# Kernel tuning notes

Measured on AMD Instinct MI355X. Metric: run time of the kernel, lower is better.

## Reference

```python
import jax, jax.numpy as jnp
import numpy as np

IMAGE_SIZE = 640
NUM_CLASSES = 80
MAX_BOXES = 100
SCORE_THR = 0.25
IOU_THR = 0.1
K_PRE = 256  # pre-NMS candidates per class (fixed-shape surrogate for tf.where filtering)
ANCHORS = np.array([[10,13],[16,30],[33,23],[30,61],[62,45],[59,119],
                    [116,90],[156,198],[373,326]], dtype=np.float32)


def setup_inputs() -> dict:
    key = jax.random.key(0)
    k5, k4, k3 = jax.random.split(key, 3)
    B = 16
    return {
        "p5": jax.random.normal(k5, (B, 20, 20, 255), dtype=jnp.float32),
        "p4": jax.random.normal(k4, (B, 40, 40, 255), dtype=jnp.float32),
        "p3": jax.random.normal(k3, (B, 80, 80, 255), dtype=jnp.float32),
    }


def _decode_layer(fm, anchors):
    # fm: [B, g, g, 3*(5+C)]; anchors: [3, 2] in input-image pixels
    B, g = fm.shape[0], fm.shape[1]
    ratio = IMAGE_SIZE / g
    fm = fm.reshape(B, g, g, 3, 5 + NUM_CLASSES)
    ctr = jax.nn.sigmoid(fm[..., :2])                      # [B,g,g,3,2]
    gx, gy = jnp.meshgrid(jnp.arange(g), jnp.arange(g))    # 'xy' indexing, same as tf
    offset = jnp.stack([gx, gy], axis=-1).astype(fm.dtype)[:, :, None, :]
    ctr = (ctr + offset) * ratio                           # pixel-space centers (x, y)
    # (anchor/ratio)*exp(t)*ratio == anchor*exp(t)
    sizes = jnp.exp(fm[..., 2:4]) * anchors                # pixel-space (w, h)
    conf = jax.nn.sigmoid(fm[..., 4:5])
    prob = jax.nn.sigmoid(fm[..., 5:])
    boxes = jnp.concatenate([ctr, sizes], axis=-1).reshape(B, -1, 4)
    scores = (conf * prob).reshape(B, -1, NUM_CLASSES)
    return boxes, scores


def _pairwise_iou(b):
    # b: [K, 4] in (x1, y1, x2, y2)
    x1, y1, x2, y2 = b[:, 0], b[:, 1], b[:, 2], b[:, 3]
    area = jnp.maximum(x2 - x1, 0.0) * jnp.maximum(y2 - y1, 0.0)
    iw = jnp.maximum(jnp.minimum(x2[:, None], x2[None, :]) - jnp.maximum(x1[:, None], x1[None, :]), 0.0)
    ih = jnp.maximum(jnp.minimum(y2[:, None], y2[None, :]) - jnp.maximum(y1[:, None], y1[None, :]), 0.0)
    inter = iw * ih
    union = area[:, None] + area[None, :] - inter
    return inter / jnp.maximum(union, 1e-9)


def _nms_class(boxes, scores):
    # boxes: [N,4], scores: [N] for one class of one image
    s = jnp.where(scores > SCORE_THR, scores, -1.0)
    top_s, top_i = jax.lax.top_k(s, K_PRE)        # score-sorted candidates
    cb = jnp.take(boxes, top_i, axis=0)           # [K_PRE, 4]
    iou = _pairwise_iou(cb)                       # [K_PRE, K_PRE]
    idx = jnp.arange(K_PRE)
    supp0 = top_s <= SCORE_THR                    # below-threshold slots start suppressed

    def body(i, supp):
        alive = ~supp[i]
        return supp | (alive & (iou[i] > IOU_THR) & (idx > i))

    supp = jax.lax.fori_loop(0, K_PRE, body, supp0)
    keep = ~supp
    # tf NMS caps output at MAX_BOXES per class (boxes are score-sorted)
    keep = keep & (jnp.cumsum(keep.astype(jnp.int32)) <= MAX_BOXES)
    kept_s = jnp.where(keep, top_s, -1.0)
    return kept_s, top_i


def _nms_image(boxes, scores):
    # boxes: [N,4], scores: [N,C]
    kept_s, top_i = jax.vmap(_nms_class, in_axes=(None, 1))(boxes, scores)  # [C,K],[C,K]
    flat_s = kept_s.reshape(-1)
    flat_i = top_i.reshape(-1)
    cls = jnp.repeat(jnp.arange(NUM_CLASSES), K_PRE)
    fs, fi = jax.lax.top_k(flat_s, MAX_BOXES)     # global top-k across all classes
    box_idx = flat_i[fi]
    valid = fs > 0.0                              # padded/suppressed slots carry -1
    out_boxes = jnp.where(valid[:, None], jnp.take(boxes, box_idx, axis=0), -1.0)
    out_scores = jnp.where(valid, fs, -1.0)
    out_labels = jnp.where(valid, cls[fi], -1).astype(jnp.int32)
    return out_boxes, out_scores, out_labels


def reference(p5, p4, p3):
    b5, s5 = _decode_layer(p5, ANCHORS[6:9])
    b4, s4 = _decode_layer(p4, ANCHORS[3:6])
    b3, s3 = _decode_layer(p3, ANCHORS[0:3])
    boxes = jnp.concatenate([b5, b4, b3], axis=1)   # [B, 25200, 4] (cx, cy, w, h)
    scores = jnp.concatenate([s5, s4, s3], axis=1)  # [B, 25200, 80]
    cx, cy, w, h = boxes[..., 0], boxes[..., 1], boxes[..., 2], boxes[..., 3]
    boxes = jnp.stack([cx - w / 2, cy - h / 2, cx + w / 2, cy + h / 2], axis=-1)
    return jax.vmap(_nms_image)(boxes, scores)      # ([B,100,4], [B,100], [B,100] int32)
```

## Files before the change

kernel.cpp:

```cpp
#include <hip/hip_runtime.h>
#include <cstdint>

#define NBOX 25200
#define NCLS 80
#define NIMG 16
#define KPRE 256
#define MAXB 100
#define SCORE_THR 0.25f
#define IOU_THR 0.1f
#define GCAP 512
#define GCAP_OLD 2048
#define NBINS_OLD 4096
#define FK 512
#define LCAP 3072
#define SCAP 24
#define CSTR 16
#define CUT 0.5f
#define BINW 0.001953125f
#define HS2 512.0f
#define RSC 262144.0f
#define BPI 394
#define FBBINS 2048

__constant__ float c_AW[9] = {10.f,16.f,33.f,30.f,62.f,59.f,116.f,156.f,373.f};
__constant__ float c_AH[9] = {13.f,30.f,23.f,61.f,45.f,119.f,90.f,198.f,326.f};

__device__ __forceinline__ float sigmoidf_(float x) { return 1.0f / (1.0f + expf(-x)); }

__device__ __forceinline__ void box_loc(int i, const float* p5, const float* p4, const float* p3,
                                        const float*& p, int& g, int& li, int& abase) {
  if (i < 1200)      { p = p5; g = 20; li = i;        abase = 6; }
  else if (i < 6000) { p = p4; g = 40; li = i - 1200; abase = 3; }
  else               { p = p3; g = 80; li = i - 6000; abase = 0; }
}

__device__ __forceinline__ float score_full(const float* p5, const float* p4, const float* p3,
                                            int b, int c, int i) {
  const float* p; int g, li, abase;
  box_loc(i, p5, p4, p3, p, g, li, abase);
  const float* f = p + (size_t)((size_t)b * g * g * 3 + li) * 85;
  return __fmul_rn(sigmoidf_(f[4]), sigmoidf_(f[5 + c]));
}

__global__ __launch_bounds__(512) void decode_push_kernel(
    const float* __restrict__ p5, const float* __restrict__ p4, const float* __restrict__ p3,
    float* __restrict__ boxes, unsigned long long* __restrict__ lists,
    uint32_t* __restrict__ cnts, uint32_t* __restrict__ ovfl)
{
  __shared__ float rec[64 * 85];
  __shared__ float conf_s[64];
  __shared__ unsigned long long slist[NCLS][SCAP];
  __shared__ uint32_t wcnt[NCLS];
  __shared__ uint32_t sbase[NCLS], sst[NCLS];

  const int bi = blockIdx.x;
  const int b = bi / BPI, r = bi - b * BPI;
  const float* p; int g, lb, s0, nb, abase;
  if (r < 19)      { p = p5; g = 20; lb = 0;    s0 = r * 64;        abase = 6; nb = 1200  - s0; }
  else if (r < 94) { p = p4; g = 40; lb = 1200; s0 = (r - 19) * 64; abase = 3; nb = 4800  - s0; }
  else             { p = p3; g = 80; lb = 6000; s0 = (r - 94) * 64; abase = 0; nb = 19200 - s0; }
  if (nb > 64) nb = 64;
  const int tid = threadIdx.x;

  {
    const float4* src4 = (const float4*)(p + ((size_t)b * g * g * 3 + s0) * 85);
    float4* rec4 = (float4*)rec;
    int n4 = nb * 85 / 4;
    for (int k = tid; k < n4; k += 512) rec4[k] = src4[k];
  }
  __syncthreads();

  if (tid < nb) {
    const float* f = rec + tid * 85;
    int li = s0 + tid;
    int cell = li / 3, a = li - cell * 3;
    float ratio = 640.0f / (float)g;
    float cx = (sigmoidf_(f[0]) + (float)(cell % g)) * ratio;
    float cy = (sigmoidf_(f[1]) + (float)(cell / g)) * ratio;
    float w = expf(f[2]) * c_AW[abase + a];
    float h = expf(f[3]) * c_AH[abase + a];
    float hw = 0.5f * w, hh = 0.5f * h;
    float4* ob = (float4*)(boxes + ((size_t)b * NBOX + lb + li) * 4);
    *ob = make_float4(cx - hw, cy - hh, cx + hw, cy + hh);
    conf_s[tid] = sigmoidf_(f[4]);
  }
  __syncthreads();

  {
    const int wave = tid >> 6, lane = tid & 63;
    const int c0 = wave * 10;
    const bool jok = lane < nb;
    const float cf = jok ? conf_s[lane] : 0.0f;
    const uint32_t gidx = (uint32_t)(lb + s0 + lane);
    const float* fl = rec + lane * 85 + 5;
    const unsigned long long lt = (lane == 0) ? 0ull : (~0ull >> (64 - lane));
    for (int cc = 0; cc < 10; ++cc) {
      int c = c0 + cc;
      float s = 0.0f;
      if (jok) s = __fmul_rn(cf, sigmoidf_(fl[c]));
      bool pred = jok && (s > CUT);
      unsigned long long m = __ballot(pred);
      uint32_t pc = (uint32_t)__popcll(m);
      if (pred) {
        uint32_t rank = (uint32_t)__popcll(m & lt);
        if (rank < SCAP)
          slist[c][rank] = ((unsigned long long)__float_as_uint(s) << 32) | (0xFFFFFFFFu - gidx);
      }
      if (lane == 0) {
        wcnt[c] = pc;
        if (pc > SCAP) ovfl[b * NCLS + c] = 1u;
      }
    }
  }
  __syncthreads();

  if (tid < NCLS) {
    uint32_t full = wcnt[tid];
    uint32_t st = full < SCAP ? full : SCAP;
    sst[tid] = st;
    sbase[tid] = atomicAdd(&cnts[(size_t)(b * NCLS + tid) * CSTR], st);
  }
  __syncthreads();

  for (int t = tid; t < NCLS * SCAP; t += 512) {
    int c = t / SCAP, k = t - c * SCAP;
    if ((uint32_t)k < sst[c]) {
      uint32_t dst = sbase[c] + (uint32_t)k;
      if (dst < LCAP)
        lists[(size_t)(b * NCLS + c) * LCAP + dst] = slist[c][k];
    }
  }
}

union ShMix2 {
  uint32_t rhist[512];
  uint32_t fhist[FBBINS];
  unsigned long long rowm[KPRE][4];
};

__global__ __launch_bounds__(512) void select_nms_list_kernel(
    const unsigned long long* __restrict__ lists, const uint32_t* __restrict__ cnts,
    const uint32_t* __restrict__ ovfl, const float* __restrict__ boxes,
    const float* __restrict__ p5, const float* __restrict__ p4, const float* __restrict__ p3,
    float* __restrict__ kept_s, int* __restrict__ top_i)
{
  const int task = blockIdx.x;
  const int b = task / NCLS, c = task - b * NCLS;
  const int tid = threadIdx.x;

  __shared__ uint32_t S[256];
  __shared__ unsigned long long keys[GCAP];
  __shared__ ShMix2 u;
  __shared__ float4 bbx[KPRE];
  __shared__ float bar_[KPRE];
  __shared__ unsigned long long suppInit[4];
  __shared__ unsigned long long sh_t[4];
  __shared__ int s_B, s_cnt, s_state, sh_stop;
  __shared__ float s_gl, s_lo, s_hi;
  __shared__ uint32_t s_above, s_g2;

  const uint32_t cntraw = cnts[(size_t)task * CSTR];
  bool fb = (ovfl[task] != 0u) || !(cntraw >= (uint32_t)KPRE && cntraw <= (uint32_t)LCAP);
  float thr = CUT;
  int n_all = (int)(cntraw < (uint32_t)LCAP ? cntraw : (uint32_t)LCAP);
  const unsigned long long* gl = lists + (size_t)task * LCAP;

  if (!fb) {
    if (tid < 256) S[tid] = 0;
    __syncthreads();
    for (int z = tid; z < n_all; z += 512) {
      float s = __uint_as_float((uint32_t)(gl[z] >> 32));
      int bin = (int)(__fmul_rn(__fsub_rn(s, CUT), HS2));
      bin = bin < 0 ? 0 : (bin > 255 ? 255 : bin);
      atomicAdd(&S[bin], 1u);
    }
    __syncthreads();
    for (int off = 1; off < 256; off <<= 1) {
      uint32_t add = 0;
      if (tid < 256 && tid + off < 256) add = S[tid + off];
      __syncthreads();
      if (tid < 256) S[tid] += add;
      __syncthreads();
    }
    if (tid == 0) s_B = 0;
    __syncthreads();
    if (tid < 256) {
      uint32_t Sz = S[tid];
      uint32_t Sz1 = (tid < 255) ? S[tid + 1] : 0u;
      if (Sz >= KPRE && (tid == 255 || Sz1 < KPRE)) s_B = tid;
    }
    __syncthreads();
    const int B = s_B;
    const uint32_t gcount = S[B];
    const uint32_t aboveB = (B < 255) ? S[B + 1] : 0u;
    thr = CUT + (float)B * BINW;
    if (gcount > 500u) {
      for (int z = tid; z < 512; z += 512) u.rhist[z] = 0u;
      __syncthreads();
      float rLo = thr;
      for (int z = tid; z < n_all; z += 512) {
        float s = __uint_as_float((uint32_t)(gl[z] >> 32));
        int bin = (int)(__fmul_rn(__fsub_rn(s, CUT), HS2));
        bin = bin < 0 ? 0 : (bin > 255 ? 255 : bin);
        if (bin == B) {
          int sub = (int)((s - rLo) * RSC);
          sub = sub < 0 ? 0 : (sub > 511 ? 511 : sub);
          atomicAdd(&u.rhist[sub], 1u);
        }
      }
      __syncthreads();
      if (tid == 0) {
        uint32_t acc = aboveB; int B2 = 0;
        for (int z = 511; z >= 0; --z) {
          acc += u.rhist[z];
          if (acc >= KPRE) { B2 = z; break; }
        }
        s_gl = rLo + (float)B2 * (BINW / 512.0f);
        s_g2 = acc;
      }
      __syncthreads();
      thr = s_gl;
      if (s_g2 > 500u) fb = true;
      __syncthreads();
    }
  }

  if (fb) {
    float lo = SCORE_THR, hi = 1.0f;
    uint32_t above = 0;
    float gl2 = SCORE_THR;
    bool done = false;
    for (int iter = 0; iter < 6 && !done; ++iter) {
      for (int z = tid; z < FBBINS; z += 512) u.fhist[z] = 0u;
      __syncthreads();
      float scale = (float)FBBINS / (hi - lo);
      for (int i = tid; i < NBOX; i += 512) {
        float s = score_full(p5, p4, p3, b, c, i);
        if (s > lo && s <= hi) {
          int bin = (int)((s - lo) * scale);
          bin = bin < 0 ? 0 : (bin > FBBINS - 1 ? FBBINS - 1 : bin);
          atomicAdd(&u.fhist[bin], 1u);
        }
      }
      __syncthreads();
      if (tid < 256) {
        uint32_t cs = 0; int base = tid * 8;
        #pragma unroll
        for (int z = 0; z < 8; ++z) cs += u.fhist[base + z];
        S[tid] = cs;
      }
      __syncthreads();
      if (tid == 0) {
        uint32_t acc = 0; int ch;
        for (ch = 255; ch >= 0; --ch) {
          if (above + acc + S[ch] >= KPRE) break;
          acc += S[ch];
        }
        if (ch < 0) { s_state = 1; s_gl = SCORE_THR; }
        else {
          int B = -1;
          for (int z = ch * 8 + 7; z >= ch * 8; --z) {
            acc += u.fhist[z];
            if (above + acc >= KPRE) { B = z; break; }
          }
          uint32_t popB = u.fhist[B];
          uint32_t aboveNew = above + acc - popB;
          float wdt = (hi - lo) / (float)FBBINS;
          float binLo = lo + (float)B * wdt;
          if (aboveNew + popB <= 496u || iter == 5) { s_state = 1; s_gl = binLo; }
          else { s_state = 0; s_lo = binLo; s_hi = binLo + wdt; s_above = aboveNew; }
        }
      }
      __syncthreads();
      if (s_state == 1) { gl2 = s_gl; done = true; }
      else { lo = s_lo; hi = s_hi; above = s_above; }
      __syncthreads();
    }
    thr = gl2;
  }

  float thr_n = __uint_as_float(__float_as_uint(thr) - 8u);

  if (tid == 0) s_cnt = 0;
  __syncthreads();
  if (!fb) {
    for (int z = tid; z < n_all; z += 512) {
      unsigned long long kk = gl[z];
      float s = __uint_as_float((uint32_t)(kk >> 32));
      if (s > thr_n) {
        int slot = atomicAdd(&s_cnt, 1);
        if (slot < GCAP) keys[slot] = kk;
      }
    }
  } else {
    for (int i = tid; i < NBOX; i += 512) {
      float s = score_full(p5, p4, p3, b, c, i);
      if (s > thr_n && s > SCORE_THR) {
        int slot = atomicAdd(&s_cnt, 1);
        if (slot < GCAP)
          keys[slot] = ((unsigned long long)__float_as_uint(s) << 32) | (0xFFFFFFFFu - (uint32_t)i);
      }
    }
  }
  __syncthreads();
  int n = s_cnt < GCAP ? s_cnt : GCAP;
  if (tid >= n) keys[tid] = 0ull;
  __syncthreads();
  for (int k = 2; k <= GCAP; k <<= 1) {
    for (int j = k >> 1; j > 0; j >>= 1) {
      int ixj = tid ^ j;
      if (ixj > tid) {
        unsigned long long a0 = keys[tid], b0_ = keys[ixj];
        bool sw = ((tid & k) == 0) ? (a0 < b0_) : (a0 > b0_);
        if (sw) { keys[tid] = b0_; keys[ixj] = a0; }
      }
      __syncthreads();
    }
  }

  const int col = tid & 255;
  float sc; int idx;
  {
    unsigned long long kk = keys[col];
    if ((uint32_t)(kk >> 32) != 0u) { sc = __uint_as_float((uint32_t)(kk >> 32)); idx = (int)(0xFFFFFFFFu - (uint32_t)kk); }
    else { sc = -1.0f; idx = 0; }
  }
  if (tid < KPRE) {
    const float* bp = boxes + ((size_t)b * NBOX + idx) * 4;
    float bx1 = bp[0], by1 = bp[1], bx2 = bp[2], by2 = bp[3];
    bbx[tid] = make_float4(bx1, by1, bx2, by2);
    bar_[tid] = __fmul_rn(fmaxf(__fsub_rn(bx2, bx1), 0.0f), fmaxf(__fsub_rn(by2, by1), 0.0f));
  }
  {
    unsigned long long alive = __ballot(sc > SCORE_THR);
    if (tid < KPRE && (tid & 63) == 0) suppInit[tid >> 6] = ~alive;
  }
  if (tid == 0) sh_stop = 0;
  __syncthreads();
  float4 MB = bbx[col];
  float x1 = MB.x, y1 = MB.y, x2 = MB.z, y2 = MB.w;
  float area = bar_[col];
  if (tid < 4) sh_t[tid] = suppInit[tid];
  __syncthreads();

  int P = 4;
  const int rg = tid >> 8;
  #pragma unroll
  for (int q = 0; q < 4; ++q) {
    for (int ii = 0; ii < 64; ii += 2) {
      int i = q * 64 + ii + rg;
      if (!((sh_t[q] >> (ii + rg)) & 1ull)) {
        float4 B = bbx[i];
        float ar = bar_[i];
        float iw = fmaxf(__fsub_rn(fminf(x2, B.z), fmaxf(x1, B.x)), 0.0f);
        float ih = fmaxf(__fsub_rn(fminf(y2, B.w), fmaxf(y1, B.y)), 0.0f);
        float inter = __fmul_rn(iw, ih);
        float ab = __fadd_rn(ar, area);
        float diff = __fsub_rn(__fmul_rn(inter, 1.1f), __fmul_rn(0.1f, ab));
        bool sup;
        if (fabsf(diff) > 1e-5f * ab) {
          sup = diff > 0.0f;
        } else {
          float uni = __fsub_rn(ab, inter);
          sup = (inter / fmaxf(uni, 1e-9f)) > IOU_THR;
        }
        sup = sup && (col > i);
        unsigned long long m = __ballot(sup);
        if ((tid & 63) == 0) u.rowm[i][(tid >> 6) & 3] = m;
      }
    }
    __syncthreads();
    if (tid == 0) {
      unsigned long long t0 = sh_t[0], t1 = sh_t[1], t2 = sh_t[2], t3 = sh_t[3];
      for (int ii = 0; ii < 64; ++ii) {
        int i = q * 64 + ii;
        unsigned long long cur = (q == 0) ? t0 : (q == 1) ? t1 : (q == 2) ? t2 : t3;
        if (!((cur >> ii) & 1ull)) {
          if (q <= 0) t0 |= u.rowm[i][0];
          if (q <= 1) t1 |= u.rowm[i][1];
          if (q <= 2) t2 |= u.rowm[i][2];
          t3 |= u.rowm[i][3];
        }
      }
      sh_t[0] = t0; sh_t[1] = t1; sh_t[2] = t2; sh_t[3] = t3;
      int kept = __popcll(~t0);
      if (q >= 1) kept += __popcll(~t1);
      if (q >= 2) kept += __popcll(~t2);
      if (q >= 3) kept += __popcll(~t3);
      if (kept >= MAXB) sh_stop = 1;
    }
    __syncthreads();
    if (sh_stop) { P = q + 1; break; }
  }

  if (tid < KPRE) {
    unsigned long long tw = sh_t[tid >> 6];
    bool kept = (tid < 64 * P) && !((tw >> (tid & 63)) & 1ull);
    int rank = 0;
    #pragma unroll
    for (int w2 = 0; w2 < 4; ++w2)
      if (w2 < (tid >> 6)) rank += __popcll(~sh_t[w2]);
    int l = tid & 63;
    rank += (l == 0) ? 0 : __popcll(~tw & ((~0ull) >> (64 - l)));
    bool fin = kept && (rank < MAXB);
    kept_s[(size_t)task * KPRE + tid] = fin ? sc : -1.0f;
    top_i[(size_t)task * KPRE + tid] = idx;
  }
}

__global__ __launch_bounds__(256) void decode_kernel(
    const float* __restrict__ p5, const float* __restrict__ p4, const float* __restrict__ p3,
    float* __restrict__ boxes, float* __restrict__ conf)
{
  int t = blockIdx.x * 256 + threadIdx.x;
  if (t >= NIMG * NBOX) return;
  int b = t / NBOX, i = t - b * NBOX;
  const float* p; int g, li, abase;
  box_loc(i, p5, p4, p3, p, g, li, abase);
  int cell = li / 3, a = li - cell * 3;
  float ratio = 640.0f / (float)g;
  const float* f = p + ((size_t)((size_t)b * g * g + cell) * 255 + a * 85);
  float cx = (sigmoidf_(f[0]) + (float)(cell % g)) * ratio;
  float cy = (sigmoidf_(f[1]) + (float)(cell / g)) * ratio;
  float w = expf(f[2]) * c_AW[abase + a];
  float h = expf(f[3]) * c_AH[abase + a];
  float hw = 0.5f * w, hh = 0.5f * h;
  float* ob = boxes + (size_t)t * 4;
  ob[0] = cx - hw; ob[1] = cy - hh; ob[2] = cx + hw; ob[3] = cy + hh;
  conf[t] = sigmoidf_(f[4]);
}

__device__ __forceinline__ float score_at(
    const float* __restrict__ p5, const float* __restrict__ p4, const float* __restrict__ p3,
    const float* __restrict__ conf, int b, int c, int i)
{
  const float* p; int g, li, abase;
  box_loc(i, p5, p4, p3, p, g, li, abase);
  float logit = p[(size_t)((size_t)b * g * g * 3 + li) * 85 + 5 + c];
  return __fmul_rn(conf[b * NBOX + i], 1.0f / (1.0f + expf(-logit)));
}

__global__ __launch_bounds__(256) void select_nms_kernel(
    const float* __restrict__ p5, const float* __restrict__ p4, const float* __restrict__ p3,
    const float* __restrict__ conf, const float* __restrict__ boxes,
    float* __restrict__ kept_s, int* __restrict__ top_i)
{
  const int task = blockIdx.x;
  const int b = task / NCLS, c = task - b * NCLS;
  const int tid = threadIdx.x;
  __shared__ uint32_t hist[NBINS_OLD];
  __shared__ uint32_t chunkS[256];
  __shared__ unsigned long long keys[GCAP_OLD];
  __shared__ float s_lo, s_hi, s_glo;
  __shared__ uint32_t s_above;
  __shared__ int s_state, s_cnt;

  float lo = SCORE_THR, hi = 1.0f;
  uint32_t above = 0;
  float gatherLo = SCORE_THR;
  bool done = false;
  for (int iter = 0; iter < 6 && !done; ++iter) {
    for (int z = tid; z < NBINS_OLD; z += 256) hist[z] = 0;
    __syncthreads();
    float scale = (float)NBINS_OLD / (hi - lo);
    for (int i = tid; i < NBOX; i += 256) {
      float s = score_at(p5, p4, p3, conf, b, c, i);
      if (s > lo && s <= hi) {
        int bin = (int)((s - lo) * scale);
        bin = bin < 0 ? 0 : (bin > NBINS_OLD - 1 ? NBINS_OLD - 1 : bin);
        atomicAdd(&hist[bin], 1u);
      }
    }
    __syncthreads();
    { uint32_t cs = 0; int base = tid * 16;
      #pragma unroll
      for (int z = 0; z < 16; ++z) cs += hist[base + z];
      chunkS[tid] = cs; }
    __syncthreads();
    if (tid == 0) {
      uint32_t acc = 0; int ch;
      for (ch = 255; ch >= 0; --ch) {
        if (above + acc + chunkS[ch] >= KPRE) break;
        acc += chunkS[ch];
      }
      if (ch < 0) { s_state = 1; s_glo = SCORE_THR; }
      else {
        int B = -1;
        for (int z = ch * 16 + 15; z >= ch * 16; --z) {
          acc += hist[z];
          if (above + acc >= KPRE) { B = z; break; }
        }
        uint32_t popB = hist[B];
        uint32_t aboveNew = above + acc - popB;
        float wdt = (hi - lo) / (float)NBINS_OLD;
        float binLo = lo + (float)B * wdt;
        if (aboveNew + popB <= 1024u || iter == 5) { s_state = 1; s_glo = binLo; }
        else { s_state = 0; s_lo = binLo; s_hi = binLo + wdt; s_above = aboveNew; }
      }
    }
    __syncthreads();
    if (s_state == 1) { gatherLo = s_glo; done = true; }
    else { lo = s_lo; hi = s_hi; above = s_above; }
    __syncthreads();
  }
  gatherLo = __uint_as_float(__float_as_uint(gatherLo) - 8u);
  if (tid == 0) s_cnt = 0;
  __syncthreads();
  for (int i = tid; i < NBOX; i += 256) {
    float s = score_at(p5, p4, p3, conf, b, c, i);
    if (s > gatherLo && s > SCORE_THR) {
      int slot = atomicAdd(&s_cnt, 1);
      if (slot < GCAP_OLD)
        keys[slot] = ((unsigned long long)__float_as_uint(s) << 32) | (uint32_t)(0xFFFFFFFFu - (uint32_t)i);
    }
  }
  __syncthreads();
  int n = s_cnt < GCAP_OLD ? s_cnt : GCAP_OLD;
  for (int z = tid; z < GCAP_OLD; z += 256) if (z >= n) keys[z] = 0ull;
  __syncthreads();
  for (int k = 2; k <= GCAP_OLD; k <<= 1) {
    for (int j = k >> 1; j > 0; j >>= 1) {
      for (int i2 = tid; i2 < GCAP_OLD; i2 += 256) {
        int ixj = i2 ^ j;
        if (ixj > i2) {
          unsigned long long a0 = keys[i2], b0_ = keys[ixj];
          bool sw = ((i2 & k) == 0) ? (a0 < b0_) : (a0 > b0_);
          if (sw) { keys[i2] = b0_; keys[ixj] = a0; }
        }
      }
      __syncthreads();
    }
  }
  __shared__ float bx1[KPRE], by1[KPRE], bx2[KPRE], by2[KPRE], bar_[KPRE], tsc[KPRE];
  __shared__ int tix[KPRE];
  __shared__ unsigned char suppA[KPRE], keepA[KPRE];
  { int r = tid;
    unsigned long long kk = keys[r];
    float sc; int idx;
    if ((uint32_t)(kk >> 32) != 0u) { sc = __uint_as_float((uint32_t)(kk >> 32)); idx = (int)(0xFFFFFFFFu - (uint32_t)kk); }
    else { sc = -1.0f; idx = 0; }
    tsc[r] = sc; tix[r] = idx;
    const float* bp = boxes + ((size_t)b * NBOX + idx) * 4;
    float x1 = bp[0], y1 = bp[1], x2 = bp[2], y2 = bp[3];
    bx1[r] = x1; by1[r] = y1; bx2[r] = x2; by2[r] = y2;
    bar_[r] = __fmul_rn(fmaxf(__fsub_rn(x2, x1), 0.0f), fmaxf(__fsub_rn(y2, y1), 0.0f));
    suppA[r] = (sc <= SCORE_THR) ? 1 : 0; }
  __syncthreads();
  for (int i = 0; i < KPRE; ++i) {
    if (suppA[i] == 0) {
      int r = tid;
      if (r > i) {
        float iw = fmaxf(__fsub_rn(fminf(bx2[r], bx2[i]), fmaxf(bx1[r], bx1[i])), 0.0f);
        float ih = fmaxf(__fsub_rn(fminf(by2[r], by2[i]), fmaxf(by1[r], by1[i])), 0.0f);
        float inter = __fmul_rn(iw, ih);
        float uni = __fsub_rn(__fadd_rn(bar_[r], bar_[i]), inter);
        float iou = inter / fmaxf(uni, 1e-9f);
        if (iou > IOU_THR) suppA[r] = 1;
      }
    }
    __syncthreads();
  }
  if (tid == 0) {
    int cnt = 0;
    for (int r = 0; r < KPRE; ++r) {
      int kp = (suppA[r] == 0) ? 1 : 0;
      if (kp && cnt < MAXB) cnt++; else kp = 0;
      keepA[r] = (unsigned char)kp;
    }
  }
  __syncthreads();
  { int r = tid;
    kept_s[(size_t)task * KPRE + r] = keepA[r] ? tsc[r] : -1.0f;
    top_i[(size_t)task * KPRE + r] = tix[r]; }
}

__global__ __launch_bounds__(256) void final_topk_kernel(
    const float* __restrict__ kept_s, const int* __restrict__ top_i,
    const float* __restrict__ boxes, float* __restrict__ out)
{
  int b = blockIdx.x, tid = threadIdx.x;
  __shared__ uint32_t hist[NBINS_OLD];
  __shared__ uint32_t chunkS[256];
  __shared__ unsigned long long keys[FK];
  __shared__ float s_lo, s_hi, s_glo;
  __shared__ uint32_t s_above;
  __shared__ int s_state, s_cnt;
  const float* ks = kept_s + (size_t)b * NCLS * KPRE;
  const int NK = NCLS * KPRE;

  float lo = SCORE_THR, hi = 1.0f;
  uint32_t above = 0;
  float gatherLo = SCORE_THR;
  bool done = false;

  for (int iter = 0; iter < 4 && !done; ++iter) {
    for (int z = tid; z < NBINS_OLD; z += 256) hist[z] = 0;
    __syncthreads();
    float scale = (float)NBINS_OLD / (hi - lo);
    for (int z = tid; z < NK; z += 256) {
      float s = ks[z];
      if (s > lo && s <= hi) {
        int bin = (int)((s - lo) * scale);
        bin = bin < 0 ? 0 : (bin > NBINS_OLD - 1 ? NBINS_OLD - 1 : bin);
        atomicAdd(&hist[bin], 1u);
      }
    }
    __syncthreads();
    {
      uint32_t cs = 0; int base = tid * 16;
      #pragma unroll
      for (int z = 0; z < 16; ++z) cs += hist[base + z];
      chunkS[tid] = cs;
    }
    __syncthreads();
    if (tid == 0) {
      uint32_t acc = 0; int ch;
      for (ch = 255; ch >= 0; --ch) {
        if (above + acc + chunkS[ch] >= MAXB) break;
        acc += chunkS[ch];
      }
      if (ch < 0) { s_state = 1; s_glo = SCORE_THR; }
      else {
        int B = -1;
        for (int z = ch * 16 + 15; z >= ch * 16; --z) {
          acc += hist[z];
          if (above + acc >= MAXB) { B = z; break; }
        }
        uint32_t popB = hist[B];
        uint32_t aboveNew = above + acc - popB;
        float wdt = (hi - lo) / (float)NBINS_OLD;
        float binLo = lo + (float)B * wdt;
        if (aboveNew + popB <= (uint32_t)(FK - 64) || iter == 3) { s_state = 1; s_glo = binLo; }
        else { s_state = 0; s_lo = binLo; s_hi = binLo + wdt; s_above = aboveNew; }
      }
    }
    __syncthreads();
    if (s_state == 1) { gatherLo = s_glo; done = true; }
    else { lo = s_lo; hi = s_hi; above = s_above; }
    __syncthreads();
  }
  gatherLo = __uint_as_float(__float_as_uint(gatherLo) - 8u);

  if (tid == 0) s_cnt = 0;
  __syncthreads();
  for (int z = tid; z < NK; z += 256) {
    float s = ks[z];
    if (s > gatherLo && s > 0.0f) {
      int slot = atomicAdd(&s_cnt, 1);
      if (slot < FK)
        keys[slot] = ((unsigned long long)__float_as_uint(s) << 32) | (uint32_t)(0xFFFFFFFFu - (uint32_t)z);
    }
  }
  __syncthreads();
  int n = s_cnt < FK ? s_cnt : FK;
  for (int z = tid; z < FK; z += 256) if (z >= n) keys[z] = 0ull;
  __syncthreads();
  for (int k = 2; k <= FK; k <<= 1) {
    for (int j = k >> 1; j > 0; j >>= 1) {
      for (int i2 = tid; i2 < FK; i2 += 256) {
        int ixj = i2 ^ j;
        if (ixj > i2) {
          unsigned long long a0 = keys[i2], b0_ = keys[ixj];
          bool sw = ((i2 & k) == 0) ? (a0 < b0_) : (a0 > b0_);
          if (sw) { keys[i2] = b0_; keys[ixj] = a0; }
        }
      }
      __syncthreads();
    }
  }
  float* ob = out + (size_t)b * MAXB * 4;
  float* os = out + (size_t)NIMG * MAXB * 4 + (size_t)b * MAXB;
  float* ol = out + (size_t)NIMG * MAXB * 4 + (size_t)NIMG * MAXB + (size_t)b * MAXB;
  for (int t = tid; t < MAXB; t += 256) {
    unsigned long long kk = keys[t];
    if ((uint32_t)(kk >> 32) != 0u) {
      float s = __uint_as_float((uint32_t)(kk >> 32));
      int fr = (int)(0xFFFFFFFFu - (uint32_t)kk);
      int cc = fr >> 8, rr = fr & 255;
      int idx = top_i[((size_t)b * NCLS + cc) * KPRE + rr];
      const float* bp = boxes + ((size_t)b * NBOX + idx) * 4;
      ob[t * 4 + 0] = bp[0]; ob[t * 4 + 1] = bp[1]; ob[t * 4 + 2] = bp[2]; ob[t * 4 + 3] = bp[3];
      os[t] = s; ol[t] = (float)cc;
    } else {
      ob[t * 4 + 0] = -1.0f; ob[t * 4 + 1] = -1.0f; ob[t * 4 + 2] = -1.0f; ob[t * 4 + 3] = -1.0f;
      os[t] = -1.0f; ol[t] = -1.0f;
    }
  }
}

extern "C" void kernel_launch(void* const* d_in, const int* in_sizes, int n_in,
                              void* d_out, int out_size, void* d_ws, size_t ws_size,
                              hipStream_t stream)
{
  const float* p5 = (const float*)d_in[0];
  const float* p4 = (const float*)d_in[1];
  const float* p3 = (const float*)d_in[2];
  float* out = (float*)d_out;

  float*    boxes = (float*)d_ws;
  float*    kept  = boxes + (size_t)NIMG * NBOX * 4;
  int*      topi  = (int*)(kept + (size_t)NIMG * NCLS * KPRE);
  uint32_t* cnts  = (uint32_t*)(topi + (size_t)NIMG * NCLS * KPRE);
  uint32_t* ovfl  = cnts + (size_t)NIMG * NCLS * CSTR;
  unsigned long long* lists = (unsigned long long*)(ovfl + NIMG * NCLS);

  size_t need_main = ((size_t)NIMG * NBOX * 4 + (size_t)NIMG * NCLS * KPRE * 2
                      + (size_t)NIMG * NCLS * CSTR + (size_t)NIMG * NCLS) * 4
                     + (size_t)NIMG * NCLS * LCAP * 8;

  if (ws_size >= need_main) {
    hipMemsetAsync(cnts, 0, (size_t)NIMG * NCLS * (CSTR + 1) * sizeof(uint32_t), stream);
    decode_push_kernel<<<NIMG * BPI, 512, 0, stream>>>(p5, p4, p3, boxes, lists, cnts, ovfl);
    select_nms_list_kernel<<<NIMG * NCLS, 512, 0, stream>>>(lists, cnts, ovfl, boxes, p5, p4, p3, kept, topi);
  } else {
    float* conf = (float*)(cnts);
    decode_kernel<<<(NIMG * NBOX + 255) / 256, 256, 0, stream>>>(p5, p4, p3, boxes, conf);
    select_nms_kernel<<<NIMG * NCLS, 256, 0, stream>>>(p5, p4, p3, conf, boxes, kept, topi);
  }
  final_topk_kernel<<<NIMG, 256, 0, stream>>>(kept, topi, boxes, out);
}
```

Measured before the change: 210.2 us.

## Prefilter class logits by threshold, compact candidates, and use shuffle bitonic sort

The decode kernel now derives a per-anchor logit threshold from the objectness confidence, so sigmoid scoring runs only on compacted candidate (lane, class) pairs instead of all 10 classes per lane. Slots are assigned with shared-memory atomics rather than ballot ranks. The NMS kernel's bitonic sort keeps keys in registers and uses wavefront shuffles for strides below 64, cutting barriers. The histogram path is also skipped when the candidate count is small. Atomic slot order changes the list order, and the -0.01 logit margin must stay conservative.

```diff
diff --git a/kernel.cpp b/kernel.cpp
--- a/kernel.cpp
+++ b/kernel.cpp
@@ -52,6 +52,7 @@
   __shared__ unsigned long long slist[NCLS][SCAP];
   __shared__ uint32_t wcnt[NCLS];
   __shared__ uint32_t sbase[NCLS], sst[NCLS];
+  __shared__ unsigned short pairbuf[8 * 64];
 
   const int bi = blockIdx.x;
   const int b = bi / BPI, r = bi - b * BPI;
@@ -62,6 +63,7 @@
   if (nb > 64) nb = 64;
   const int tid = threadIdx.x;
 
+  if (tid < NCLS) wcnt[tid] = 0;
   {
     const float4* src4 = (const float4*)(p + ((size_t)b * g * g * 3 + s0) * 85);
     float4* rec4 = (float4*)rec;
@@ -90,32 +92,55 @@
     const int wave = tid >> 6, lane = tid & 63;
     const int c0 = wave * 10;
     const bool jok = lane < nb;
-    const float cf = jok ? conf_s[lane] : 0.0f;
-    const uint32_t gidx = (uint32_t)(lb + s0 + lane);
+    float cl = jok ? rec[lane * 85 + 4] : -1.0f;
+    float Lthr;
+    if (!jok || cl <= 0.0f) {
+      Lthr = 3.0e38f;
+    } else {
+      float conf = conf_s[lane];
+      float u = CUT / conf;
+      if (u > 0.999f) Lthr = -3.0e38f;
+      else Lthr = logf(u / (1.0f - u)) - 0.01f;
+    }
     const float* fl = rec + lane * 85 + 5;
     const unsigned long long lt = (lane == 0) ? 0ull : (~0ull >> (64 - lane));
+    unsigned short* pb = pairbuf + (wave << 6);
+
+    auto flushFn = [&](int mm) {
+      if (lane < mm) {
+        int e = pb[lane];
+        int l2 = e >> 4, cc2 = e & 15;
+        int c2 = c0 + cc2;
+        float s = __fmul_rn(conf_s[l2], sigmoidf_(rec[l2 * 85 + 5 + c2]));
+        if (s > CUT) {
+          uint32_t slot = atomicAdd(&wcnt[c2], 1u);
+          if (slot < SCAP)
+            slist[c2][slot] = ((unsigned long long)__float_as_uint(s) << 32)
+                              | (0xFFFFFFFFu - (uint32_t)(lb + s0 + l2));
+        }
+      }
+    };
+
+    int m = 0;
     for (int cc = 0; cc < 10; ++cc) {
-      int c = c0 + cc;
-      float s = 0.0f;
-      if (jok) s = __fmul_rn(cf, sigmoidf_(fl[c]));
-      bool pred = jok && (s > CUT);
-      unsigned long long m = __ballot(pred);
-      uint32_t pc = (uint32_t)__popcll(m);
-      if (pred) {
-        uint32_t rank = (uint32_t)__popcll(m & lt);
-        if (rank < SCAP)
-          slist[c][rank] = ((unsigned long long)__float_as_uint(s) << 32) | (0xFFFFFFFFu - gidx);
-      }
-      if (lane == 0) {
-        wcnt[c] = pc;
-        if (pc > SCAP) ovfl[b * NCLS + c] = 1u;
-      }
-    }
+      float lg = jok ? fl[c0 + cc] : -3.0e38f;
+      bool cand = lg > Lthr;
+      unsigned long long mk = __ballot(cand);
+      int pc = __popcll(mk);
+      if (m + pc > 64) { flushFn(m); m = 0; }
+      if (cand) {
+        int rank = __popcll(mk & lt);
+        pb[m + rank] = (unsigned short)((lane << 4) | cc);
+      }
+      m += pc;
+    }
+    flushFn(m);
   }
   __syncthreads();
 
   if (tid < NCLS) {
     uint32_t full = wcnt[tid];
+    if (full > SCAP) ovfl[b * NCLS + tid] = 1u;
     uint32_t st = full < SCAP ? full : SCAP;
     sst[tid] = st;
     sbase[tid] = atomicAdd(&cnts[(size_t)(b * NCLS + tid) * CSTR], st);
@@ -165,7 +190,7 @@
   int n_all = (int)(cntraw < (uint32_t)LCAP ? cntraw : (uint32_t)LCAP);
   const unsigned long long* gl = lists + (size_t)task * LCAP;
 
-  if (!fb) {
+  if (!fb && n_all > 500) {
     if (tid < 256) S[tid] = 0;
     __syncthreads();
     for (int z = tid; z < n_all; z += 512) {
@@ -306,17 +331,26 @@
   int n = s_cnt < GCAP ? s_cnt : GCAP;
   if (tid >= n) keys[tid] = 0ull;
   __syncthreads();
-  for (int k = 2; k <= GCAP; k <<= 1) {
-    for (int j = k >> 1; j > 0; j >>= 1) {
-      int ixj = tid ^ j;
-      if (ixj > tid) {
-        unsigned long long a0 = keys[tid], b0_ = keys[ixj];
-        bool sw = ((tid & k) == 0) ? (a0 < b0_) : (a0 > b0_);
-        if (sw) { keys[tid] = b0_; keys[ixj] = a0; }
-      }
-      __syncthreads();
-    }
-  }
+  {
+    unsigned long long v = keys[tid];
+    for (int k = 2; k <= GCAP; k <<= 1) {
+      for (int j = k >> 1; j > 0; j >>= 1) {
+        unsigned long long pv;
+        if (j >= 64) {
+          keys[tid] = v;
+          __syncthreads();
+          pv = keys[tid ^ j];
+          __syncthreads();
+        } else {
+          pv = __shfl_xor(v, j, 64);
+        }
+        bool takeMax = (((tid & k) == 0) == ((tid & j) == 0));
+        v = takeMax ? (v > pv ? v : pv) : (v < pv ? v : pv);
+      }
+    }
+    keys[tid] = v;
+  }
+  __syncthreads();
 
   const int col = tid & 255;
   float sc; int idx;
```

Result: no change. 209.9 us (-0.1%).
